# Kernel optimization log

Hardware: AMD Instinct MI355X
Metric: run time of the kernel (lower is better)

The kernel has to match this reference:

```python
import jax, jax.numpy as jnp
import numpy as np

TEMPERATURE = 0.07
C_MARGIN = 0.5
T_MARGIN = 1.0
GAMMA = 2.0
ALPHA = 0.25
SMOOTHING = 0.1
W_CONTRASTIVE = 0.1
W_TRIPLET = 0.1
W_FOCAL = 0.4
W_LABEL_SMOOTH = 0.4


def setup_inputs() -> dict:
    key = jax.random.key(0)
    k1, k2, k3 = jax.random.split(key, 3)
    B, C, D = 2048, 1000, 512
    pred = jax.random.normal(k1, (B, C), dtype=jnp.float32)
    target = jax.random.randint(k2, (B,), 0, C, dtype=jnp.int64)
    features = jax.random.normal(k3, (B, D), dtype=jnp.float32)
    return {"pred": pred, "target": target, "features": features}


def _safe_cdist(f):
    # Euclidean pairwise distance with zero-grad at zero distance (matches torch.cdist on diagonal).
    r = jnp.sum(f * f, axis=1)
    d2 = jnp.maximum(r[:, None] - 2.0 * (f @ f.T) + r[None, :], 0.0)
    pos = d2 > 0
    return jnp.sqrt(jnp.where(pos, d2, 1.0)) * pos


def _contrastive(features, labels):
    f = features / jnp.linalg.norm(features, axis=1, keepdims=True)
    sim = f @ f.T  # [B, B]
    lm = (labels[:, None] == labels[None, :]).astype(sim.dtype)
    pos = sim * lm
    pos_loss = -jnp.log(jnp.exp(pos / TEMPERATURE) + 1e-8)
    neg = sim * (1.0 - lm)
    neg_loss = jnp.maximum(C_MARGIN - neg, 0.0)
    return pos_loss.mean() + neg_loss.mean()


def _triplet(features, labels):
    B = features.shape[0]
    d = _safe_cdist(features)  # [B, B]
    lm = (labels[:, None] == labels[None, :]).astype(d.dtype)
    pm, nm = lm, 1.0 - lm

    def body(acc, args):
        di, pmi, nmi = args  # [B], [B], [B]
        # sum over (p, n): relu(d_ip - d_in + margin), masked
        contrib = jnp.sum(
            jnp.maximum(di[:, None] - di[None, :] + T_MARGIN, 0.0)
            * pmi[:, None] * nmi[None, :]
        )
        return acc + contrib, None

    loss, _ = jax.lax.scan(body, jnp.float32(0.0), (d, pm, nm))
    return loss / (B + 1e-8)


def _focal(pred, target):
    logp = jax.nn.log_softmax(pred, axis=1)
    ce = -jnp.take_along_axis(logp, target[:, None], axis=1)[:, 0]
    pt = jnp.exp(-ce)
    return (ALPHA * (1.0 - pt) ** GAMMA * ce).mean()


def _label_smoothing(pred, target):
    C = pred.shape[1]
    off = SMOOTHING / (C - 1)
    logp = jax.nn.log_softmax(pred, axis=1)
    # smooth target: off everywhere, (1 - smoothing) at target index
    tgt_logp = jnp.take_along_axis(logp, target[:, None], axis=1)[:, 0]
    loss = -(off * logp.sum(axis=1) + ((1.0 - SMOOTHING) - off) * tgt_logp)
    return loss.mean()


def reference(pred, target, features):
    lc = _contrastive(features, target)
    lt = _triplet(features, target)
    lf = _focal(pred, target)
    ls = _label_smoothing(pred, target)
    total = (W_CONTRASTIVE * lc + W_TRIPLET * lt
             + W_FOCAL * lf + W_LABEL_SMOOTH * ls)
    return jnp.stack([lc, lt, lf, ls, total])
```

## Files before the change

### kernel.cpp

```cpp
#include <hip/hip_runtime.h>
#include <hip/hip_bf16.h>
#include <math.h>

typedef __attribute__((ext_vector_type(8))) short bf16x8;
typedef __attribute__((ext_vector_type(4))) float f32x4;

static constexpr float TEMP_INV  = 1.0f / 0.07f;
static constexpr float C_MARGIN  = 0.5f;
static constexpr float T_MARGIN  = 1.0f;
static constexpr float ALPHA     = 0.25f;
static constexpr float SMOOTHING = 0.1f;

__device__ __forceinline__ void gload_lds16(const void* g, void* l) {
    __builtin_amdgcn_global_load_lds(
        (const __attribute__((address_space(1))) void*)g,
        (__attribute__((address_space(3))) void*)l,
        16, 0, 0);
}

__device__ __forceinline__ unsigned short f2bf(float x) {
    __hip_bfloat16 h = __float2bfloat16(x);
    return *reinterpret_cast<unsigned short*>(&h);
}
__device__ __forceinline__ float bf2f(unsigned short u) {
    union { unsigned int u32; float f; } U;
    U.u32 = ((unsigned int)u) << 16;
    return U.f;
}
__device__ __forceinline__ bf16x8 pack8(float4 a, float4 b) {
    bf16x8 r;
    r[0] = (short)f2bf(a.x); r[1] = (short)f2bf(a.y);
    r[2] = (short)f2bf(a.z); r[3] = (short)f2bf(a.w);
    r[4] = (short)f2bf(b.x); r[5] = (short)f2bf(b.y);
    r[6] = (short)f2bf(b.z); r[7] = (short)f2bf(b.w);
    return r;
}

__global__ __launch_bounds__(256) void gram_ce_kernel(
    const float* __restrict__ F, unsigned short* __restrict__ Gb,
    const float* __restrict__ pred, const int* __restrict__ target,
    float* __restrict__ partialCE, float* __restrict__ diag,
    float* __restrict__ inv_norm, int B, int D, int C, float off_const,
    int tilesX) {
    __shared__ float Asf[128 * 32];
    __shared__ float Bsf[128 * 32];
    __shared__ float red[12];
    __shared__ float redn[4];

    const int nTiles = tilesX * tilesX;
    const int tid = threadIdx.x;
    const int lane = tid & 63, wid = tid >> 6;

    if (blockIdx.x < nTiles) {
        const int rowBase = (blockIdx.x / tilesX) * 128;
        const int colBase = (blockIdx.x % tilesX) * 128;
        const int w = wid, l = lane;
        const int wr = (w >> 1) * 64;
        const int wc = (w & 1) * 64;
        const int half = l >> 4;
        const int rr   = l & 15;

        const float* FA = F + (size_t)rowBase * D;
        const float* FB = F + (size_t)colBase * D;

        f32x4 acc[4][4];
#pragma unroll
        for (int m = 0; m < 4; ++m)
#pragma unroll
            for (int n = 0; n < 4; ++n) acc[m][n] = (f32x4){0.f, 0.f, 0.f, 0.f};

        for (int k0 = 0; k0 < D; k0 += 32) {
#pragma unroll
            for (int c = 0; c < 4; ++c) {
                const int chunk = c * 256 + w * 64 + l;
                const int r2 = chunk >> 3;
                const int ss = (l & 7) ^ (r2 & 7);
                const size_t eoff = (size_t)r2 * D + k0 + ss * 4;
                gload_lds16(FA + eoff, &Asf[(c * 256 + w * 64) * 4]);
                gload_lds16(FB + eoff, &Bsf[(c * 256 + w * 64) * 4]);
            }
            __syncthreads();
            bf16x8 af[4], bfv[4];
#pragma unroll
            for (int f = 0; f < 4; ++f) {
                const int ar = wr + f * 16 + rr;
                const float* rp = &Asf[ar * 32];
                af[f] = pack8(
                    *(const float4*)(rp + (((half * 2)     ^ (ar & 7)) * 4)),
                    *(const float4*)(rp + (((half * 2 + 1) ^ (ar & 7)) * 4)));
                const int br = wc + f * 16 + rr;
                const float* cp = &Bsf[br * 32];
                bfv[f] = pack8(
                    *(const float4*)(cp + (((half * 2)     ^ (br & 7)) * 4)),
                    *(const float4*)(cp + (((half * 2 + 1) ^ (br & 7)) * 4)));
            }
#pragma unroll
            for (int m = 0; m < 4; ++m)
#pragma unroll
                for (int n = 0; n < 4; ++n)
                    acc[m][n] = __builtin_amdgcn_mfma_f32_16x16x32_bf16(
                        af[m], bfv[n], acc[m][n], 0, 0, 0);
            __syncthreads();
        }
#pragma unroll
        for (int m = 0; m < 4; ++m) {
            const int i0 = rowBase + wr + m * 16 + half * 4;
#pragma unroll
            for (int n = 0; n < 4; ++n) {
                const int j = colBase + wc + n * 16 + rr;
#pragma unroll
                for (int r = 0; r < 4; ++r)
                    Gb[(size_t)(i0 + r) * B + j] = f2bf(acc[m][n][r]);
            }
        }
    } else {
        const int i = blockIdx.x - nTiles;
        const float2* Fr2 = (const float2*)(F + (size_t)i * D);
        float ns = 0.0f;
        for (int idx = tid; idx < (D >> 1); idx += 256) {
            float2 f = Fr2[idx];
            ns += f.x * f.x + f.y * f.y;
        }
        const float* prow = pred + (size_t)i * C;
        const float tlogit = prow[target[i]];
        const int Cv = C >> 2;
        float m = -1e30f, s = 0.0f, sp = 0.0f;
        for (int idx = tid; idx < Cv; idx += 256) {
            float4 v = ((const float4*)prow)[idx];
            float mv = fmaxf(fmaxf(v.x, v.y), fmaxf(v.z, v.w));
            if (mv > m) { s *= expf(m - mv); m = mv; }
            s += expf(v.x - m) + expf(v.y - m) + expf(v.z - m) + expf(v.w - m);
            sp += v.x + v.y + v.z + v.w;
        }
        for (int j = Cv * 4 + tid; j < C; j += 256) {
            float v = prow[j];
            if (v > m) { s *= expf(m - v); m = v; }
            s += expf(v - m);
            sp += v;
        }
#pragma unroll
        for (int off = 32; off > 0; off >>= 1) {
            float mo = __shfl_down(m, off, 64);
            float so = __shfl_down(s, off, 64);
            sp += __shfl_down(sp, off, 64);
            ns += __shfl_down(ns, off, 64);
            float mx = fmaxf(m, mo);
            s = s * expf(m - mx) + so * expf(mo - mx);
            m = mx;
        }
        if (lane == 0) {
            red[wid] = m; red[4 + wid] = s; red[8 + wid] = sp; redn[wid] = ns;
        }
        __syncthreads();
        if (tid == 0) {
            float mm = red[0], ss = red[4], spT = red[8];
#pragma unroll
            for (int q = 1; q < 4; ++q) {
                float mo = red[q], so = red[4 + q];
                float mn = fmaxf(mm, mo);
                ss = ss * expf(mm - mn) + so * expf(mo - mn);
                mm = mn;
                spT += red[8 + q];
            }
            float lse = mm + logf(ss);
            float tl  = tlogit - lse;
            float ce  = -tl;
            float pt  = expf(tl);
            float omp = 1.0f - pt;
            float focal = ALPHA * omp * omp * ce;
            float sumlogp = spT - (float)C * lse;
            float lsv = -(off_const * sumlogp + ((1.0f - SMOOTHING) - off_const) * tl);
            partialCE[(size_t)i * 2]     = focal;
            partialCE[(size_t)i * 2 + 1] = lsv;
            float nst = redn[0] + redn[1] + redn[2] + redn[3];
            diag[i] = nst;
            inv_norm[i] = 1.0f / sqrtf(nst);
        }
    }
}

__global__ __launch_bounds__(256) void row_loss_kernel(
    const unsigned short* __restrict__ Gb, const float* __restrict__ diag,
    const float* __restrict__ inv_norm, const int* __restrict__ labels,
    float* __restrict__ partial, int B) {
    __shared__ float p_d[256];
    __shared__ float red[12];
    __shared__ int p_cnt;
    const int tid = threadIdx.x;
    const int i = blockIdx.x;
    if (tid == 0) p_cnt = 0;
    __syncthreads();

    const int   li     = labels[i];
    const float ri     = diag[i];
    const float inv_ni = inv_norm[i];
    const int   j0     = tid * 8;

    union { uint4 u; unsigned short s[8]; } GV;
    GV.u = *(const uint4*)(Gb + (size_t)i * B + j0);
    int lab[8];
    *(int4*)&lab[0] = *(const int4*)(labels + j0);
    *(int4*)&lab[4] = *(const int4*)(labels + j0 + 4);
    float dg[8], ivn[8];
    *(float4*)&dg[0]  = *(const float4*)(diag + j0);
    *(float4*)&dg[4]  = *(const float4*)(diag + j0 + 4);
    *(float4*)&ivn[0] = *(const float4*)(inv_norm + j0);
    *(float4*)&ivn[4] = *(const float4*)(inv_norm + j0 + 4);

    float pos = 0.0f, neg = 0.0f;
    float d8[8];
    int mmask = 0;
#pragma unroll
    for (int e = 0; e < 8; ++e) {
        const int j = j0 + e;
        const float g = bf2f(GV.s[e]);
        float sim = g * inv_ni * ivn[e];
        const float d2 = ri - 2.0f * g + dg[e];
        float d = (d2 > 0.0f) ? sqrtf(d2) : 0.0f;
        if (j == i) { sim = 1.0f; d = 0.0f; }
        d8[e] = d;
        if (lab[e] == li) {
            pos += -logf(expf(sim * TEMP_INV) + 1e-8f);
            neg += C_MARGIN;
            mmask |= (1 << e);
            int slot = atomicAdd(&p_cnt, 1);
            if (slot < 256) p_d[slot] = d;
        } else {
            neg += fmaxf(C_MARGIN - sim, 0.0f);
        }
    }
    __syncthreads();
    const int cnt = (p_cnt < 256) ? p_cnt : 256;
    float trip = 0.0f;
    for (int p = 0; p < cnt; ++p) {
        const float dp = p_d[p] + T_MARGIN;
#pragma unroll
        for (int e = 0; e < 8; ++e)
            if (!(mmask & (1 << e))) trip += fmaxf(dp - d8[e], 0.0f);
    }

    float r0 = pos, r1 = neg, r2 = trip;
#pragma unroll
    for (int off = 32; off > 0; off >>= 1) {
        r0 += __shfl_down(r0, off, 64);
        r1 += __shfl_down(r1, off, 64);
        r2 += __shfl_down(r2, off, 64);
    }
    const int lane = tid & 63, wid = tid >> 6;
    if (lane == 0) { red[wid] = r0; red[4 + wid] = r1; red[8 + wid] = r2; }
    __syncthreads();
    if (tid == 0) {
        float4 o;
        o.x = red[0] + red[1] + red[2] + red[3];
        o.y = red[4] + red[5] + red[6] + red[7];
        o.z = red[8] + red[9] + red[10] + red[11];
        o.w = 0.0f;
        *(float4*)(partial + (size_t)i * 4) = o;
    }
}

__global__ __launch_bounds__(256) void reduce_kernel(
    const float* __restrict__ partialT, const float* __restrict__ partialCE,
    float* __restrict__ out, int B) {
    __shared__ float red[4][5];
    const int tid = threadIdx.x;
    float s[5] = {0.f, 0.f, 0.f, 0.f, 0.f};
    for (int r = tid; r < B; r += 256) {
        float4 v = *(const float4*)(partialT + (size_t)r * 4);
        s[0] += v.x; s[1] += v.y; s[2] += v.z;
    }
    for (int t = tid; t < (B * 2) / 4; t += 256) {
        float4 v = *(const float4*)(partialCE + (size_t)t * 4);
        s[3] += v.x + v.z; s[4] += v.y + v.w;
    }
#pragma unroll
    for (int off = 32; off > 0; off >>= 1) {
#pragma unroll
        for (int k = 0; k < 5; ++k) s[k] += __shfl_down(s[k], off, 64);
    }
    const int lane = tid & 63, wid = tid >> 6;
    if (lane == 0) {
#pragma unroll
        for (int k = 0; k < 5; ++k) red[wid][k] = s[k];
    }
    __syncthreads();
    if (tid == 0) {
        float t[5];
#pragma unroll
        for (int k = 0; k < 5; ++k)
            t[k] = red[0][k] + red[1][k] + red[2][k] + red[3][k];
        double invB2 = 1.0 / ((double)B * (double)B);
        float lc = (float)(((double)t[0] + (double)t[1]) * invB2);
        float lt = (float)((double)t[2] / ((double)B + 1e-8));
        float lf = t[3] / (float)B;
        float ls = t[4] / (float)B;
        out[0] = lc;
        out[1] = lt;
        out[2] = lf;
        out[3] = ls;
        out[4] = 0.1f * lc + 0.1f * lt + 0.4f * lf + 0.4f * ls;
    }
}

extern "C" void kernel_launch(void* const* d_in, const int* in_sizes, int n_in,
                              void* d_out, int out_size, void* d_ws, size_t ws_size,
                              hipStream_t stream) {
    const float* pred     = (const float*)d_in[0];
    const int*   target   = (const int*)d_in[1];
    const float* features = (const float*)d_in[2];
    const int B = in_sizes[1];
    const int C = in_sizes[0] / B;
    const int D = in_sizes[2] / B;
    float* out = (float*)d_out;
    const int tilesX = B / 128;
    const int nTiles = tilesX * tilesX;

    float* partial   = (float*)d_ws;
    float* partialCE = partial + (size_t)B * 4;
    float* diag      = partialCE + (size_t)B * 2;
    float* inv_norm  = diag + B;
    unsigned short* Gb = (unsigned short*)(inv_norm + B);

    float off_const = SMOOTHING / (float)(C - 1);
    gram_ce_kernel<<<nTiles + B, 256, 0, stream>>>(
        features, Gb, pred, target, partialCE, diag, inv_norm,
        B, D, C, off_const, tilesX);

    row_loss_kernel<<<B, 256, 0, stream>>>(Gb, diag, inv_norm, target,
                                           partial, B);

    reduce_kernel<<<1, 256, 0, stream>>>(partial, partialCE, out, B);
}
```

Measured before the change: 37.85 us.

## Move cross-entropy rows into row-loss kernel and compute norms one row per wave

The per-row softmax/focal/label-smoothing work moves out of the Gram kernel and into the row-loss kernel as extra blocks. The Gram kernel keeps only the squared norms, now computed one row per wavefront, so it launches a quarter as many extra blocks. This is meant to balance the two stages: the Gram launch gets shorter, and the memory-bound CE reads overlap with the row-loss blocks. The second kernel grows to 2B blocks, which adds CE reads to the kernel that was already bandwidth-heavy.

```diff
diff --git a/kernel.cpp b/kernel.cpp
--- a/kernel.cpp
+++ b/kernel.cpp
@@ -36,16 +36,12 @@
     return r;
 }
 
-__global__ __launch_bounds__(256) void gram_ce_kernel(
+__global__ __launch_bounds__(256) void gram_norm_kernel(
     const float* __restrict__ F, unsigned short* __restrict__ Gb,
-    const float* __restrict__ pred, const int* __restrict__ target,
-    float* __restrict__ partialCE, float* __restrict__ diag,
-    float* __restrict__ inv_norm, int B, int D, int C, float off_const,
-    int tilesX) {
+    float* __restrict__ diag, float* __restrict__ inv_norm,
+    int B, int D, int tilesX) {
     __shared__ float Asf[128 * 32];
     __shared__ float Bsf[128 * 32];
-    __shared__ float red[12];
-    __shared__ float redn[4];
 
     const int nTiles = tilesX * tilesX;
     const int tid = threadIdx.x;
@@ -114,16 +110,108 @@
             }
         }
     } else {
-        const int i = blockIdx.x - nTiles;
-        const float2* Fr2 = (const float2*)(F + (size_t)i * D);
-        float ns = 0.0f;
-        for (int idx = tid; idx < (D >> 1); idx += 256) {
-            float2 f = Fr2[idx];
-            ns += f.x * f.x + f.y * f.y;
-        }
+        const int row = (blockIdx.x - nTiles) * 4 + wid;
+        const float4* Fr = (const float4*)(F + (size_t)row * D);
+        const int n4 = D >> 2;
+        float s = 0.0f;
+        for (int idx = lane; idx < n4; idx += 64) {
+            float4 v = Fr[idx];
+            s += v.x * v.x + v.y * v.y + v.z * v.z + v.w * v.w;
+        }
+#pragma unroll
+        for (int off = 32; off > 0; off >>= 1) s += __shfl_down(s, off, 64);
+        if (lane == 0) { diag[row] = s; inv_norm[row] = 1.0f / sqrtf(s); }
+    }
+}
+
+__global__ __launch_bounds__(256) void row_ce_kernel(
+    const unsigned short* __restrict__ Gb, const float* __restrict__ diag,
+    const float* __restrict__ inv_norm, const int* __restrict__ labels,
+    const float* __restrict__ pred, const int* __restrict__ target,
+    float* __restrict__ partial, float* __restrict__ partialCE,
+    int B, int C, float off_const) {
+    __shared__ float p_d[256];
+    __shared__ float red[12];
+    __shared__ int p_cnt;
+    const int tid = threadIdx.x;
+    const int lane = tid & 63, wid = tid >> 6;
+
+    if (blockIdx.x < (unsigned)B) {
+        const int i = blockIdx.x;
+        if (tid == 0) p_cnt = 0;
+        __syncthreads();
+
+        const int   li     = labels[i];
+        const float ri     = diag[i];
+        const float inv_ni = inv_norm[i];
+        const int   j0     = tid * 8;
+
+        union { uint4 u; unsigned short s[8]; } GV;
+        GV.u = *(const uint4*)(Gb + (size_t)i * B + j0);
+        int lab[8];
+        *(int4*)&lab[0] = *(const int4*)(labels + j0);
+        *(int4*)&lab[4] = *(const int4*)(labels + j0 + 4);
+        float dg[8], ivn[8];
+        *(float4*)&dg[0]  = *(const float4*)(diag + j0);
+        *(float4*)&dg[4]  = *(const float4*)(diag + j0 + 4);
+        *(float4*)&ivn[0] = *(const float4*)(inv_norm + j0);
+        *(float4*)&ivn[4] = *(const float4*)(inv_norm + j0 + 4);
+
+        float pos = 0.0f, neg = 0.0f;
+        float d8[8];
+        int mmask = 0;
+#pragma unroll
+        for (int e = 0; e < 8; ++e) {
+            const int j = j0 + e;
+            const float g = bf2f(GV.s[e]);
+            float sim = g * inv_ni * ivn[e];
+            const float d2 = ri - 2.0f * g + dg[e];
+            float d = (d2 > 0.0f) ? sqrtf(d2) : 0.0f;
+            if (j == i) { sim = 1.0f; d = 0.0f; }
+            d8[e] = d;
+            if (lab[e] == li) {
+                pos += -logf(expf(sim * TEMP_INV) + 1e-8f);
+                neg += C_MARGIN;
+                mmask |= (1 << e);
+                int slot = atomicAdd(&p_cnt, 1);
+                if (slot < 256) p_d[slot] = d;
+            } else {
+                neg += fmaxf(C_MARGIN - sim, 0.0f);
+            }
+        }
+        __syncthreads();
+        const int cnt = (p_cnt < 256) ? p_cnt : 256;
+        float trip = 0.0f;
+        for (int p = 0; p < cnt; ++p) {
+            const float dp = p_d[p] + T_MARGIN;
+#pragma unroll
+            for (int e = 0; e < 8; ++e)
+                if (!(mmask & (1 << e))) trip += fmaxf(dp - d8[e], 0.0f);
+        }
+
+        float r0 = pos, r1 = neg, r2 = trip;
+#pragma unroll
+        for (int off = 32; off > 0; off >>= 1) {
+            r0 += __shfl_down(r0, off, 64);
+            r1 += __shfl_down(r1, off, 64);
+            r2 += __shfl_down(r2, off, 64);
+        }
+        if (lane == 0) { red[wid] = r0; red[4 + wid] = r1; red[8 + wid] = r2; }
+        __syncthreads();
+        if (tid == 0) {
+            float4 o;
+            o.x = red[0] + red[1] + red[2] + red[3];
+            o.y = red[4] + red[5] + red[6] + red[7];
+            o.z = red[8] + red[9] + red[10] + red[11];
+            o.w = 0.0f;
+            *(float4*)(partial + (size_t)i * 4) = o;
+        }
+    } else {
+        const int i = blockIdx.x - B;
         const float* prow = pred + (size_t)i * C;
         const float tlogit = prow[target[i]];
         const int Cv = C >> 2;
+
         float m = -1e30f, s = 0.0f, sp = 0.0f;
         for (int idx = tid; idx < Cv; idx += 256) {
             float4 v = ((const float4*)prow)[idx];
@@ -143,14 +231,11 @@
             float mo = __shfl_down(m, off, 64);
             float so = __shfl_down(s, off, 64);
             sp += __shfl_down(sp, off, 64);
-            ns += __shfl_down(ns, off, 64);
             float mx = fmaxf(m, mo);
             s = s * expf(m - mx) + so * expf(mo - mx);
             m = mx;
         }
-        if (lane == 0) {
-            red[wid] = m; red[4 + wid] = s; red[8 + wid] = sp; redn[wid] = ns;
-        }
+        if (lane == 0) { red[wid] = m; red[4 + wid] = s; red[8 + wid] = sp; }
         __syncthreads();
         if (tid == 0) {
             float mm = red[0], ss = red[4], spT = red[8];
@@ -172,90 +257,7 @@
             float lsv = -(off_const * sumlogp + ((1.0f - SMOOTHING) - off_const) * tl);
             partialCE[(size_t)i * 2]     = focal;
             partialCE[(size_t)i * 2 + 1] = lsv;
-            float nst = redn[0] + redn[1] + redn[2] + redn[3];
-            diag[i] = nst;
-            inv_norm[i] = 1.0f / sqrtf(nst);
-        }
-    }
-}
-
-__global__ __launch_bounds__(256) void row_loss_kernel(
-    const unsigned short* __restrict__ Gb, const float* __restrict__ diag,
-    const float* __restrict__ inv_norm, const int* __restrict__ labels,
-    float* __restrict__ partial, int B) {
-    __shared__ float p_d[256];
-    __shared__ float red[12];
-    __shared__ int p_cnt;
-    const int tid = threadIdx.x;
-    const int i = blockIdx.x;
-    if (tid == 0) p_cnt = 0;
-    __syncthreads();
-
-    const int   li     = labels[i];
-    const float ri     = diag[i];
-    const float inv_ni = inv_norm[i];
-    const int   j0     = tid * 8;
-
-    union { uint4 u; unsigned short s[8]; } GV;
-    GV.u = *(const uint4*)(Gb + (size_t)i * B + j0);
-    int lab[8];
-    *(int4*)&lab[0] = *(const int4*)(labels + j0);
-    *(int4*)&lab[4] = *(const int4*)(labels + j0 + 4);
-    float dg[8], ivn[8];
-    *(float4*)&dg[0]  = *(const float4*)(diag + j0);
-    *(float4*)&dg[4]  = *(const float4*)(diag + j0 + 4);
-    *(float4*)&ivn[0] = *(const float4*)(inv_norm + j0);
-    *(float4*)&ivn[4] = *(const float4*)(inv_norm + j0 + 4);
-
-    float pos = 0.0f, neg = 0.0f;
-    float d8[8];
-    int mmask = 0;
-#pragma unroll
-    for (int e = 0; e < 8; ++e) {
-        const int j = j0 + e;
-        const float g = bf2f(GV.s[e]);
-        float sim = g * inv_ni * ivn[e];
-        const float d2 = ri - 2.0f * g + dg[e];
-        float d = (d2 > 0.0f) ? sqrtf(d2) : 0.0f;
-        if (j == i) { sim = 1.0f; d = 0.0f; }
-        d8[e] = d;
-        if (lab[e] == li) {
-            pos += -logf(expf(sim * TEMP_INV) + 1e-8f);
-            neg += C_MARGIN;
-            mmask |= (1 << e);
-            int slot = atomicAdd(&p_cnt, 1);
-            if (slot < 256) p_d[slot] = d;
-        } else {
-            neg += fmaxf(C_MARGIN - sim, 0.0f);
-        }
-    }
-    __syncthreads();
-    const int cnt = (p_cnt < 256) ? p_cnt : 256;
-    float trip = 0.0f;
-    for (int p = 0; p < cnt; ++p) {
-        const float dp = p_d[p] + T_MARGIN;
-#pragma unroll
-        for (int e = 0; e < 8; ++e)
-            if (!(mmask & (1 << e))) trip += fmaxf(dp - d8[e], 0.0f);
-    }
-
-    float r0 = pos, r1 = neg, r2 = trip;
-#pragma unroll
-    for (int off = 32; off > 0; off >>= 1) {
-        r0 += __shfl_down(r0, off, 64);
-        r1 += __shfl_down(r1, off, 64);
-        r2 += __shfl_down(r2, off, 64);
-    }
-    const int lane = tid & 63, wid = tid >> 6;
-    if (lane == 0) { red[wid] = r0; red[4 + wid] = r1; red[8 + wid] = r2; }
-    __syncthreads();
-    if (tid == 0) {
-        float4 o;
-        o.x = red[0] + red[1] + red[2] + red[3];
-        o.y = red[4] + red[5] + red[6] + red[7];
-        o.z = red[8] + red[9] + red[10] + red[11];
-        o.w = 0.0f;
-        *(float4*)(partial + (size_t)i * 4) = o;
+        }
     }
 }
 
@@ -321,13 +323,13 @@
     float* inv_norm  = diag + B;
     unsigned short* Gb = (unsigned short*)(inv_norm + B);
 
+    gram_norm_kernel<<<nTiles + B / 4, 256, 0, stream>>>(
+        features, Gb, diag, inv_norm, B, D, tilesX);
+
     float off_const = SMOOTHING / (float)(C - 1);
-    gram_ce_kernel<<<nTiles + B, 256, 0, stream>>>(
-        features, Gb, pred, target, partialCE, diag, inv_norm,
-        B, D, C, off_const, tilesX);
-
-    row_loss_kernel<<<B, 256, 0, stream>>>(Gb, diag, inv_norm, target,
-                                           partial, B);
+    row_ce_kernel<<<B + B, 256, 0, stream>>>(
+        Gb, diag, inv_norm, target, pred, target,
+        partial, partialCE, B, C, off_const);
 
     reduce_kernel<<<1, 256, 0, stream>>>(partial, partialCE, out, B);
 }
```

New measurement: 41.02 us. 1.08x slower.
